# Optimization experiments

Hardware: AMD Instinct MI355X
Metric: run time of the kernel (lower is better)

Reference implementation:

```python
import jax, jax.numpy as jnp
import numpy as np

B, S, H, D = 2, 2048, 16, 64


def setup_inputs() -> dict:
    key = jax.random.key(0)
    kq, kk, kv, km = jax.random.split(key, 4)
    q = jax.random.normal(kq, (B, S, H, D), dtype=jnp.float32)
    k = jax.random.normal(kk, (B, S, H, D), dtype=jnp.float32)
    v = jax.random.normal(kv, (B, S, H, D), dtype=jnp.float32)
    pattern_mask = jax.random.bernoulli(km, 0.1, (S, S))
    return {"q": q, "k": k, "v": v, "pattern_mask": pattern_mask}


def reference(q, k, v, pattern_mask):
    # Faithful math of the torch module: for each query row i, attend only to
    # columns j where pattern_mask[i, j]; softmax over the selected columns
    # per (batch, head); rows with no selected columns produce zeros.
    head_dim = q.shape[-1]
    scale = 1.0 / jnp.sqrt(jnp.asarray(head_dim, dtype=q.dtype))
    # scores: [B, H, S_q, S_k]
    scores = jnp.einsum('bihd,bjhd->bhij', q, k) * scale
    neg = jnp.finfo(scores.dtype).min
    masked = jnp.where(pattern_mask[None, None, :, :], scores, neg)
    attn = jax.nn.softmax(masked, axis=-1)
    # zero out rows with no active columns (softmax over all-masked row is uniform garbage)
    row_has = jnp.any(pattern_mask, axis=-1)  # [S]
    attn = jnp.where(row_has[None, None, :, None], attn, jnp.zeros((), dtype=attn.dtype))
    # output: [B, S, H, D]
    out = jnp.einsum('bhij,bjhd->bihd', attn, v)
    return out
```

## Files before the change

### kernel.cpp

```cpp
#include <hip/hip_runtime.h>
#include <hip/hip_bf16.h>
#include <math.h>

#define SLEN 2048
#define NBATCH 2
#define NH 16
#define DH 64
#define WPR 64
#define NROUND 32
#define TILEB 16384
#define CONVBLK (NBATCH * NH * NROUND)
#define PACKBLK (SLEN * WPR / 256)

typedef __attribute__((ext_vector_type(4))) short short4v;
typedef __attribute__((ext_vector_type(8))) short short8v;
typedef __attribute__((ext_vector_type(4))) float float4v;
typedef __attribute__((ext_vector_type(16))) float float16v;

__device__ __forceinline__ unsigned short f2bf(float f) {
  unsigned u = __float_as_uint(f);
  u += 0x7fffu + ((u >> 16) & 1u);
  return (unsigned short)(u >> 16);
}

__device__ __forceinline__ float fexp2(float x) {
#if __has_builtin(__builtin_amdgcn_exp2f)
  return __builtin_amdgcn_exp2f(x);
#else
  return __expf(x * 0.6931471805599453f);
#endif
}

__device__ __forceinline__ unsigned pack_bf2(float a, float b) {
  unsigned ua = __float_as_uint(a); ua += 0x7fffu + ((ua >> 16) & 1u);
  unsigned ub = __float_as_uint(b); ub += 0x7fffu + ((ub >> 16) & 1u);
  return __builtin_amdgcn_perm(ub, ua, 0x07060302u);
}

__device__ __forceinline__ unsigned cvtpk(float lo, float hi) {
  unsigned r;
  asm("v_cvt_pk_bf16_f32 %0, %1, %2" : "=v"(r) : "v"(lo), "v"(hi));
  return r;
}

__device__ __forceinline__ unsigned nib4(unsigned w) {
  return ((w * 0x01020408u) >> 24) & 0xFu;
}

__global__ __launch_bounds__(256) void prep_kernel(
    const float* __restrict__ kk, const float* __restrict__ vv,
    const void* __restrict__ mask,
    char* __restrict__ img, unsigned* __restrict__ packed, int convblocks) {
  const int tid = threadIdx.x;
  if (blockIdx.x >= convblocks) {
    const int w = (blockIdx.x - convblocks) * 256 + tid;
    const uint4* bp = (const uint4*)((const char*)mask + (size_t)w * 32);
    uint4 x = bp[0], y = bp[1];
    const unsigned orw = (x.x | x.y) | (x.z | x.w) | (y.x | y.y) | (y.z | y.w);
    __shared__ int s0, sm;
    if (tid == 0) { s0 = 0; sm = 0; }
    __syncthreads();
    const int lane0 = ((tid & 63) == 0);
    if (__any((orw & 0x000000ffu) != 0) && lane0) atomicOr(&s0, 1);
    if (__any((orw & 0xffffff00u) != 0) && lane0) atomicOr(&sm, 1);
    __syncthreads();
    unsigned bits;
    if (s0 && sm) {
      bits = nib4(x.x) | (nib4(x.y) << 4) | (nib4(x.z) << 8) | (nib4(x.w) << 12) |
             (nib4(y.x) << 16) | (nib4(y.y) << 20) | (nib4(y.z) << 24) | (nib4(y.w) << 28);
    } else {
      const unsigned* m = (const unsigned*)mask + (size_t)w * 32;
      bits = 0u;
#pragma unroll
      for (int j = 0; j < 32; j++) bits |= (m[j] ? 1u : 0u) << j;
    }
    packed[w] = bits;
    return;
  }
  const int bid = blockIdx.x;
  const int t = bid & 31;
  const int bh = bid >> 5;
  const int b = bh >> 4, h = bh & 15;
  char* timg = img + (size_t)bid * TILEB;

  {
    const int r = tid >> 2;
    const int dg = (tid & 3) << 4;
    const float* src = kk + (((size_t)(b * SLEN + t * 64 + r) * NH + h) * DH + dg);
    const int f = ((r >> 5) << 2) + (dg >> 4);
    char* base = timg + f * 1024 + (r & 31) * 16;
    float4v x0 = *(const float4v*)(src);
    float4v x1 = *(const float4v*)(src + 4);
    float4v x2 = *(const float4v*)(src + 8);
    float4v x3 = *(const float4v*)(src + 12);
    union { unsigned u[4]; short8v s8; } lo, hi;
    lo.u[0] = pack_bf2(x0.x, x0.y); lo.u[1] = pack_bf2(x0.z, x0.w);
    lo.u[2] = pack_bf2(x1.x, x1.y); lo.u[3] = pack_bf2(x1.z, x1.w);
    hi.u[0] = pack_bf2(x2.x, x2.y); hi.u[1] = pack_bf2(x2.z, x2.w);
    hi.u[2] = pack_bf2(x3.x, x3.y); hi.u[3] = pack_bf2(x3.z, x3.w);
    *(short8v*)(base) = lo.s8;
    *(short8v*)(base + 512) = hi.s8;
  }
  {
    __shared__ unsigned short vlds[64 * 68];
    const int key = tid >> 2;
    const int dg = (tid & 3) << 4;
    const float* src = vv + (((size_t)(b * SLEN + t * 64 + key) * NH + h) * DH + dg);
    unsigned short* lp = vlds + key * 68 + dg;
#pragma unroll
    for (int i = 0; i < 4; i++) {
      float4v x = *(const float4v*)(src + i * 4);
      union { unsigned u[2]; short4v s4; } cv;
      cv.u[0] = pack_bf2(x.x, x.y);
      cv.u[1] = pack_bf2(x.z, x.w);
      *(short4v*)(lp + i * 4) = cv.s4;
    }
    __syncthreads();
#pragma unroll
    for (int c = 0; c < 2; c++) {
      const int cell = c * 256 + tid;
      const int fp = cell >> 6;
      const int lane16 = cell & 63;
      const int d = ((fp >> 2) & 1) * 32 + (lane16 & 31);
      const int pbase = 32 * ((fp >> 1) & 1) + 16 * (fp & 1) + 4 * (lane16 >> 5);
      union { unsigned short s[8]; short8v v8; } w;
#pragma unroll
      for (int slot = 0; slot < 8; slot++) {
        const int p = pbase + 8 * (slot >> 2) + (slot & 3);
        w.s[slot] = vlds[p * 68 + d];
      }
      *(short8v*)(timg + (8 + fp) * 1024 + lane16 * 16) = w.v8;
    }
  }
}

__global__ __launch_bounds__(256, 2) void sattn_fast13(
    const float* __restrict__ q, const unsigned* __restrict__ pmask,
    const char* __restrict__ img, float* __restrict__ out) {
  const int tid = threadIdx.x;
  const int xcd = blockIdx.x & 7;
  const int j = blockIdx.x >> 3;
  const int bh = xcd * 4 + (j >> 4);
  const int chunk = j & 15;
  const int b = bh >> 4;
  const int hd = bh & 15;
  const int wave = tid >> 6;
  const int lane = tid & 63;
  const int l31 = lane & 31;
  const int hl = lane >> 5;

  const int qrow = chunk * 128 + wave * 32 + l31;
  const int qw = qrow * WPR;

  const float SCL2 = 0.18033688011112042f;
  short8v qf[4];
  {
    const float* qp = q + (((size_t)b * SLEN + qrow) * NH + hd) * DH;
#pragma unroll
    for (int ds = 0; ds < 4; ds++) {
      float4v x0 = *(const float4v*)(qp + ds * 16 + hl * 8);
      float4v x1 = *(const float4v*)(qp + ds * 16 + hl * 8 + 4);
      union { unsigned u[4]; short8v s8; } cv;
      cv.u[0] = pack_bf2(x0.x * SCL2, x0.y * SCL2);
      cv.u[1] = pack_bf2(x0.z * SCL2, x0.w * SCL2);
      cv.u[2] = pack_bf2(x1.x * SCL2, x1.y * SCL2);
      cv.u[3] = pack_bf2(x1.z * SCL2, x1.w * SCL2);
      qf[ds] = cv.s8;
    }
  }

  const char* fb0 = img + (size_t)bh * (NROUND * TILEB) + lane * 16;
  const char* fb1 = fb0 + 4096;
  const char* fb2 = fb0 + 8192;
  const char* fb3 = fb0 + 12288;

  float16v acc0 = {}, acc1 = {};
  float lsum = 0.f;

  short8v kf0 = *(const short8v*)(fb0 + 0);
  short8v kf1 = *(const short8v*)(fb0 + 1024);
  short8v kf2 = *(const short8v*)(fb0 + 2048);
  short8v kf3 = *(const short8v*)(fb0 + 3072);
  short8v kf4 = *(const short8v*)(fb1 + 0);
  short8v kf5 = *(const short8v*)(fb1 + 1024);
  short8v kf6 = *(const short8v*)(fb1 + 2048);
  short8v kf7 = *(const short8v*)(fb1 + 3072);
  short8v vf0 = *(const short8v*)(fb2 + 0);
  short8v vf1 = *(const short8v*)(fb2 + 1024);
  short8v vf2 = *(const short8v*)(fb2 + 2048);
  short8v vf3 = *(const short8v*)(fb2 + 3072);
  short8v vf4 = *(const short8v*)(fb3 + 0);
  short8v vf5 = *(const short8v*)(fb3 + 1024);
  short8v vf6 = *(const short8v*)(fb3 + 2048);
  short8v vf7 = *(const short8v*)(fb3 + 3072);
  uint2 m = *(const uint2*)&pmask[qw];

  for (int t = 0; t < NROUND; t++) {
    const unsigned m0 = m.x, m1 = m.y;
    const int tn = (t + 1 < NROUND) ? t + 1 : t;

    __builtin_amdgcn_s_setprio(1);
    float16v st0 = {}, st1 = {};
    st0 = __builtin_amdgcn_mfma_f32_32x32x16_bf16(kf0, qf[0], st0, 0, 0, 0);
    st1 = __builtin_amdgcn_mfma_f32_32x32x16_bf16(kf4, qf[0], st1, 0, 0, 0);
    st0 = __builtin_amdgcn_mfma_f32_32x32x16_bf16(kf1, qf[1], st0, 0, 0, 0);
    st1 = __builtin_amdgcn_mfma_f32_32x32x16_bf16(kf5, qf[1], st1, 0, 0, 0);
    st0 = __builtin_amdgcn_mfma_f32_32x32x16_bf16(kf2, qf[2], st0, 0, 0, 0);
    st1 = __builtin_amdgcn_mfma_f32_32x32x16_bf16(kf6, qf[2], st1, 0, 0, 0);
    st0 = __builtin_amdgcn_mfma_f32_32x32x16_bf16(kf3, qf[3], st0, 0, 0, 0);
    st1 = __builtin_amdgcn_mfma_f32_32x32x16_bf16(kf7, qf[3], st1, 0, 0, 0);
    __builtin_amdgcn_s_setprio(0);

    const int adv = (tn != t) ? TILEB : 0;
    fb0 += adv; fb1 += adv; fb2 += adv; fb3 += adv;
    kf0 = *(const short8v*)(fb0 + 0);
    kf1 = *(const short8v*)(fb0 + 1024);
    kf2 = *(const short8v*)(fb0 + 2048);
    kf3 = *(const short8v*)(fb0 + 3072);
    kf4 = *(const short8v*)(fb1 + 0);
    kf5 = *(const short8v*)(fb1 + 1024);
    kf6 = *(const short8v*)(fb1 + 2048);
    kf7 = *(const short8v*)(fb1 + 3072);
    m = *(const uint2*)&pmask[qw + 2 * tn];

    float p0[16], p1[16];
#pragma unroll
    for (int u = 0; u < 4; u++) {
      const unsigned hw0 = m0 >> (8 * u + 4 * hl);
      const unsigned hw1 = m1 >> (8 * u + 4 * hl);
      {
        float a0 = fexp2(st0[4 * u + 0]); a0 = (hw0 & 1u) ? a0 : 0.f;
        float a1 = fexp2(st0[4 * u + 1]); a1 = (hw0 & 2u) ? a1 : 0.f;
        float a2 = fexp2(st0[4 * u + 2]); a2 = (hw0 & 4u) ? a2 : 0.f;
        float a3 = fexp2(st0[4 * u + 3]); a3 = (hw0 & 8u) ? a3 : 0.f;
        lsum += (a0 + a1) + (a2 + a3);
        p0[4 * u + 0] = a0; p0[4 * u + 1] = a1; p0[4 * u + 2] = a2; p0[4 * u + 3] = a3;
      }
      {
        float a0 = fexp2(st1[4 * u + 0]); a0 = (hw1 & 1u) ? a0 : 0.f;
        float a1 = fexp2(st1[4 * u + 1]); a1 = (hw1 & 2u) ? a1 : 0.f;
        float a2 = fexp2(st1[4 * u + 2]); a2 = (hw1 & 4u) ? a2 : 0.f;
        float a3 = fexp2(st1[4 * u + 3]); a3 = (hw1 & 8u) ? a3 : 0.f;
        lsum += (a0 + a1) + (a2 + a3);
        p1[4 * u + 0] = a0; p1[4 * u + 1] = a1; p1[4 * u + 2] = a2; p1[4 * u + 3] = a3;
      }
    }
    short8v pf0, pf1, pf2, pf3;
    {
      union { unsigned u[4]; short8v s8; } c0, c1, c2, c3;
#pragma unroll
      for (int jj = 0; jj < 4; jj++) {
        c0.u[jj] = cvtpk(p0[2 * jj], p0[2 * jj + 1]);
        c1.u[jj] = cvtpk(p0[8 + 2 * jj], p0[8 + 2 * jj + 1]);
        c2.u[jj] = cvtpk(p1[2 * jj], p1[2 * jj + 1]);
        c3.u[jj] = cvtpk(p1[8 + 2 * jj], p1[8 + 2 * jj + 1]);
      }
      pf0 = c0.s8; pf1 = c1.s8; pf2 = c2.s8; pf3 = c3.s8;
    }

    __builtin_amdgcn_s_setprio(1);
    acc0 = __builtin_amdgcn_mfma_f32_32x32x16_bf16(vf0, pf0, acc0, 0, 0, 0);
    acc1 = __builtin_amdgcn_mfma_f32_32x32x16_bf16(vf4, pf0, acc1, 0, 0, 0);
    acc0 = __builtin_amdgcn_mfma_f32_32x32x16_bf16(vf1, pf1, acc0, 0, 0, 0);
    acc1 = __builtin_amdgcn_mfma_f32_32x32x16_bf16(vf5, pf1, acc1, 0, 0, 0);
    acc0 = __builtin_amdgcn_mfma_f32_32x32x16_bf16(vf2, pf2, acc0, 0, 0, 0);
    acc1 = __builtin_amdgcn_mfma_f32_32x32x16_bf16(vf6, pf2, acc1, 0, 0, 0);
    acc0 = __builtin_amdgcn_mfma_f32_32x32x16_bf16(vf3, pf3, acc0, 0, 0, 0);
    acc1 = __builtin_amdgcn_mfma_f32_32x32x16_bf16(vf7, pf3, acc1, 0, 0, 0);
    __builtin_amdgcn_s_setprio(0);

    vf0 = *(const short8v*)(fb2 + 0);
    vf1 = *(const short8v*)(fb2 + 1024);
    vf2 = *(const short8v*)(fb2 + 2048);
    vf3 = *(const short8v*)(fb2 + 3072);
    vf4 = *(const short8v*)(fb3 + 0);
    vf5 = *(const short8v*)(fb3 + 1024);
    vf6 = *(const short8v*)(fb3 + 2048);
    vf7 = *(const short8v*)(fb3 + 3072);
  }

  lsum += __shfl_xor(lsum, 32);
  const float inv = (lsum > 0.f) ? 1.f / lsum : 0.f;
  float* op = out + (((size_t)b * SLEN + qrow) * NH + hd) * DH;
#pragma unroll
  for (int u = 0; u < 4; u++) {
    float4v o0, o1;
    o0.x = acc0[4 * u + 0] * inv; o0.y = acc0[4 * u + 1] * inv;
    o0.z = acc0[4 * u + 2] * inv; o0.w = acc0[4 * u + 3] * inv;
    o1.x = acc1[4 * u + 0] * inv; o1.y = acc1[4 * u + 1] * inv;
    o1.z = acc1[4 * u + 2] * inv; o1.w = acc1[4 * u + 3] * inv;
    *(float4v*)(op + 8 * u + 4 * hl) = o0;
    *(float4v*)(op + 32 + 8 * u + 4 * hl) = o1;
  }
}

__global__ __launch_bounds__(256) void sattn_fallback(
    const float* __restrict__ q, const float* __restrict__ kk,
    const float* __restrict__ vv, const unsigned int* __restrict__ pmask,
    float* __restrict__ out) {
  __shared__ __align__(16) unsigned short Kt[16 * 64];
  __shared__ __align__(16) unsigned short Vt[64 * 20];

  const int tid = threadIdx.x;
  const int chunk = blockIdx.x & 31;
  const int bh = blockIdx.x >> 5;
  const int b = bh >> 4;
  const int h = bh & 15;
  const int wave = tid >> 6;
  const int lane = tid & 63;
  const int lq = lane & 15;
  const int g = lane >> 4;

  const int qrow = chunk * 64 + wave * 16 + lq;

  short4v qf[4];
  {
    const float* qp = q + (((size_t)b * SLEN + qrow) * NH + h) * DH;
#pragma unroll
    for (int ks = 0; ks < 4; ks++) {
      float4v x = *(const float4v*)(qp + ks * 16 + g * 4);
      short4v s;
      s.x = (short)f2bf(x.x); s.y = (short)f2bf(x.y);
      s.z = (short)f2bf(x.z); s.w = (short)f2bf(x.w);
      qf[ks] = s;
    }
  }

  const int srow = tid >> 4;
  const int scol = (tid & 15) * 4;
  const size_t kvbase = (size_t)b * SLEN * (NH * DH) + (size_t)h * DH;

  float4v acc[4] = {};
  float m_run = -INFINITY;
  float l_run = 0.f;

  for (int t = 0; t < SLEN / 16; t++) {
    const int kbase = t * 16;
    __syncthreads();
    {
      const size_t rowoff = kvbase + (size_t)(kbase + srow) * (NH * DH) + scol;
      float4v x = *(const float4v*)(kk + rowoff);
      short4v s;
      s.x = (short)f2bf(x.x); s.y = (short)f2bf(x.y);
      s.z = (short)f2bf(x.z); s.w = (short)f2bf(x.w);
      const int off = (scol * 2) ^ ((srow & 7) << 4);
      *(short4v*)((char*)Kt + srow * 128 + off) = s;

      float4v y = *(const float4v*)(vv + rowoff);
      Vt[(scol + 0) * 20 + srow] = f2bf(y.x);
      Vt[(scol + 1) * 20 + srow] = f2bf(y.y);
      Vt[(scol + 2) * 20 + srow] = f2bf(y.z);
      Vt[(scol + 3) * 20 + srow] = f2bf(y.w);
    }
    __syncthreads();

    float4v stv = {0.f, 0.f, 0.f, 0.f};
#pragma unroll
    for (int ks = 0; ks < 4; ks++) {
      const int off = ((ks * 16 + g * 4) * 2) ^ ((lq & 7) << 4);
      short4v kf = *(const short4v*)((const char*)Kt + lq * 128 + off);
      stv = __builtin_amdgcn_mfma_f32_16x16x16bf16_1k(kf, qf[ks], stv, 0, 0, 0);
    }

    const unsigned int mw = pmask[qrow * WPR + (kbase >> 5)];
    const int shift = (kbase & 16) + g * 4;
    float sc[4];
    float tmax = -INFINITY;
#pragma unroll
    for (int r = 0; r < 4; r++) {
      bool a = (mw >> (shift + r)) & 1u;
      sc[r] = a ? stv[r] * 0.125f : -INFINITY;
      tmax = fmaxf(tmax, sc[r]);
    }
    tmax = fmaxf(tmax, __shfl_xor(tmax, 16));
    tmax = fmaxf(tmax, __shfl_xor(tmax, 32));
    const float mnew = fmaxf(m_run, tmax);
    const float muse = (mnew > -1e37f) ? mnew : 0.f;
    const float alpha = __expf(m_run - muse);
    float p[4], tsum = 0.f;
#pragma unroll
    for (int r = 0; r < 4; r++) {
      p[r] = __expf(sc[r] - muse);
      tsum += p[r];
    }
    tsum += __shfl_xor(tsum, 16);
    tsum += __shfl_xor(tsum, 32);
    l_run = l_run * alpha + tsum;
    m_run = mnew;

    short4v pfv;
    pfv.x = (short)f2bf(p[0]); pfv.y = (short)f2bf(p[1]);
    pfv.z = (short)f2bf(p[2]); pfv.w = (short)f2bf(p[3]);

#pragma unroll
    for (int n = 0; n < 4; n++) {
      acc[n][0] *= alpha; acc[n][1] *= alpha;
      acc[n][2] *= alpha; acc[n][3] *= alpha;
      short4v vf = *(const short4v*)((const char*)Vt + ((n * 16 + lq) * 20 + g * 4) * 2);
      acc[n] = __builtin_amdgcn_mfma_f32_16x16x16bf16_1k(vf, pfv, acc[n], 0, 0, 0);
    }
  }

  const float inv = (l_run > 0.f) ? 1.f / l_run : 0.f;
  float* op = out + (((size_t)b * SLEN + qrow) * NH + h) * DH;
#pragma unroll
  for (int n = 0; n < 4; n++) {
    float4v o;
    o.x = acc[n][0] * inv; o.y = acc[n][1] * inv;
    o.z = acc[n][2] * inv; o.w = acc[n][3] * inv;
    *(float4v*)(op + n * 16 + g * 4) = o;
  }
}

extern "C" void kernel_launch(void* const* d_in, const int* in_sizes, int n_in,
                              void* d_out, int out_size, void* d_ws, size_t ws_size,
                              hipStream_t stream) {
  const float* q = (const float*)d_in[0];
  const float* k = (const float*)d_in[1];
  const float* v = (const float*)d_in[2];
  const void* mask = d_in[3];
  float* out = (float*)d_out;

  unsigned int* packed = (unsigned int*)((char*)d_ws + 256);
  char* img = (char*)d_ws + (1 << 20);
  const size_t need = (size_t)(1 << 20) + (size_t)CONVBLK * TILEB;

  if (ws_size >= need) {
    prep_kernel<<<CONVBLK + PACKBLK, 256, 0, stream>>>(k, v, mask, img, packed, CONVBLK);
    sattn_fast13<<<NBATCH * NH * (SLEN / 128), 256, 0, stream>>>(q, packed, img, out);
  } else {
    prep_kernel<<<PACKBLK, 256, 0, stream>>>(k, v, mask, nullptr, packed, 0);
    sattn_fallback<<<NBATCH * NH * (SLEN / 64), 256, 0, stream>>>(q, k, v, packed, out);
  }
}
```

Measured before the change: 66.70 us.

## Stage K/V tiles in a shared LDS ring via async global-to-LDS loads

The attention kernel now runs 512-thread blocks that each cover 256 query rows. Previously every wave streamed its own copy of the pre-swizzled K/V tiles from global memory into registers. Now the whole block cooperatively copies groups of four tiles into a double-buffered 128KB LDS ring using direct global-to-LDS loads, and waves read their MFMA fragments from LDS. This cuts redundant L2/global traffic and overlaps the fetch of the next group with compute on the current one. The cost is a large LDS footprint that allows only one block per CU, a barrier per group, and LDS read latency that is no longer hidden by register prefetch. Whether the barrier waits for the async LDS loads depends on compiler-inserted waitcnts.

```diff
diff --git a/kernel.cpp b/kernel.cpp
--- a/kernel.cpp
+++ b/kernel.cpp
@@ -16,6 +16,9 @@
 typedef __attribute__((ext_vector_type(8))) short short8v;
 typedef __attribute__((ext_vector_type(4))) float float4v;
 typedef __attribute__((ext_vector_type(16))) float float16v;
+
+typedef __attribute__((address_space(1))) void gas_void;
+typedef __attribute__((address_space(3))) void las_void;
 
 __device__ __forceinline__ unsigned short f2bf(float f) {
   unsigned u = __float_as_uint(f);
@@ -134,14 +137,16 @@
   }
 }
 
-__global__ __launch_bounds__(256, 2) void sattn_fast13(
+__global__ __launch_bounds__(512, 2) void sattn_fast14(
     const float* __restrict__ q, const unsigned* __restrict__ pmask,
     const char* __restrict__ img, float* __restrict__ out) {
+  __shared__ __align__(16) char ring[8 * TILEB];
+
   const int tid = threadIdx.x;
   const int xcd = blockIdx.x & 7;
   const int j = blockIdx.x >> 3;
-  const int bh = xcd * 4 + (j >> 4);
-  const int chunk = j & 15;
+  const int bh = xcd * 4 + (j >> 3);
+  const int chunk = j & 7;
   const int b = bh >> 4;
   const int hd = bh & 15;
   const int wave = tid >> 6;
@@ -149,7 +154,7 @@
   const int l31 = lane & 31;
   const int hl = lane >> 5;
 
-  const int qrow = chunk * 128 + wave * 32 + l31;
+  const int qrow = chunk * 256 + wave * 32 + l31;
   const int qw = qrow * WPR;
 
   const float SCL2 = 0.18033688011112042f;
@@ -169,114 +174,118 @@
     }
   }
 
-  const char* fb0 = img + (size_t)bh * (NROUND * TILEB) + lane * 16;
-  const char* fb1 = fb0 + 4096;
-  const char* fb2 = fb0 + 8192;
-  const char* fb3 = fb0 + 12288;
+  const char* gimg = img + (size_t)bh * (NROUND * TILEB) + tid * 16;
 
   float16v acc0 = {}, acc1 = {};
   float lsum = 0.f;
 
-  short8v kf0 = *(const short8v*)(fb0 + 0);
-  short8v kf1 = *(const short8v*)(fb0 + 1024);
-  short8v kf2 = *(const short8v*)(fb0 + 2048);
-  short8v kf3 = *(const short8v*)(fb0 + 3072);
-  short8v kf4 = *(const short8v*)(fb1 + 0);
-  short8v kf5 = *(const short8v*)(fb1 + 1024);
-  short8v kf6 = *(const short8v*)(fb1 + 2048);
-  short8v kf7 = *(const short8v*)(fb1 + 3072);
-  short8v vf0 = *(const short8v*)(fb2 + 0);
-  short8v vf1 = *(const short8v*)(fb2 + 1024);
-  short8v vf2 = *(const short8v*)(fb2 + 2048);
-  short8v vf3 = *(const short8v*)(fb2 + 3072);
-  short8v vf4 = *(const short8v*)(fb3 + 0);
-  short8v vf5 = *(const short8v*)(fb3 + 1024);
-  short8v vf6 = *(const short8v*)(fb3 + 2048);
-  short8v vf7 = *(const short8v*)(fb3 + 3072);
-  uint2 m = *(const uint2*)&pmask[qw];
-
-  for (int t = 0; t < NROUND; t++) {
-    const unsigned m0 = m.x, m1 = m.y;
-    const int tn = (t + 1 < NROUND) ? t + 1 : t;
-
-    __builtin_amdgcn_s_setprio(1);
-    float16v st0 = {}, st1 = {};
-    st0 = __builtin_amdgcn_mfma_f32_32x32x16_bf16(kf0, qf[0], st0, 0, 0, 0);
-    st1 = __builtin_amdgcn_mfma_f32_32x32x16_bf16(kf4, qf[0], st1, 0, 0, 0);
-    st0 = __builtin_amdgcn_mfma_f32_32x32x16_bf16(kf1, qf[1], st0, 0, 0, 0);
-    st1 = __builtin_amdgcn_mfma_f32_32x32x16_bf16(kf5, qf[1], st1, 0, 0, 0);
-    st0 = __builtin_amdgcn_mfma_f32_32x32x16_bf16(kf2, qf[2], st0, 0, 0, 0);
-    st1 = __builtin_amdgcn_mfma_f32_32x32x16_bf16(kf6, qf[2], st1, 0, 0, 0);
-    st0 = __builtin_amdgcn_mfma_f32_32x32x16_bf16(kf3, qf[3], st0, 0, 0, 0);
-    st1 = __builtin_amdgcn_mfma_f32_32x32x16_bf16(kf7, qf[3], st1, 0, 0, 0);
-    __builtin_amdgcn_s_setprio(0);
-
-    const int adv = (tn != t) ? TILEB : 0;
-    fb0 += adv; fb1 += adv; fb2 += adv; fb3 += adv;
-    kf0 = *(const short8v*)(fb0 + 0);
-    kf1 = *(const short8v*)(fb0 + 1024);
-    kf2 = *(const short8v*)(fb0 + 2048);
-    kf3 = *(const short8v*)(fb0 + 3072);
-    kf4 = *(const short8v*)(fb1 + 0);
-    kf5 = *(const short8v*)(fb1 + 1024);
-    kf6 = *(const short8v*)(fb1 + 2048);
-    kf7 = *(const short8v*)(fb1 + 3072);
-    m = *(const uint2*)&pmask[qw + 2 * tn];
-
-    float p0[16], p1[16];
+#pragma unroll
+  for (int i = 0; i < 4; i++) {
+    char* dst = &ring[i * TILEB] + tid * 16;
+    const char* src = gimg + (size_t)i * TILEB;
+    __builtin_amdgcn_global_load_lds((gas_void*)(src), (las_void*)(dst), 16, 0, 0);
+    __builtin_amdgcn_global_load_lds((gas_void*)(src + 8192), (las_void*)(dst + 8192), 16, 0, 0);
+  }
+  __syncthreads();
+
+  for (int g = 0; g < 8; g++) {
+    if (g < 7) {
+      const int dstbase = ((g + 1) & 1) * 4;
+#pragma unroll
+      for (int i = 0; i < 4; i++) {
+        const int tn = 4 * g + 4 + i;
+        char* dst = &ring[(dstbase + i) * TILEB] + tid * 16;
+        const char* src = gimg + (size_t)tn * TILEB;
+        __builtin_amdgcn_global_load_lds((gas_void*)(src), (las_void*)(dst), 16, 0, 0);
+        __builtin_amdgcn_global_load_lds((gas_void*)(src + 8192), (las_void*)(dst + 8192), 16, 0, 0);
+      }
+    }
+
 #pragma unroll
     for (int u = 0; u < 4; u++) {
-      const unsigned hw0 = m0 >> (8 * u + 4 * hl);
-      const unsigned hw1 = m1 >> (8 * u + 4 * hl);
+      const int t = 4 * g + u;
+      const char* Kl = &ring[((g & 1) * 4 + u) * TILEB] + lane * 16;
+      const char* Vl = Kl + 8192;
+      const uint2 m = *(const uint2*)&pmask[qw + 2 * t];
+      const unsigned m0 = m.x, m1 = m.y;
+
+      short8v kf0 = *(const short8v*)(Kl + 0);
+      short8v kf1 = *(const short8v*)(Kl + 1024);
+      short8v kf2 = *(const short8v*)(Kl + 2048);
+      short8v kf3 = *(const short8v*)(Kl + 3072);
+      short8v kf4 = *(const short8v*)(Kl + 4096);
+      short8v kf5 = *(const short8v*)(Kl + 5120);
+      short8v kf6 = *(const short8v*)(Kl + 6144);
+      short8v kf7 = *(const short8v*)(Kl + 7168);
+
+      __builtin_amdgcn_s_setprio(1);
+      float16v st0 = {}, st1 = {};
+      st0 = __builtin_amdgcn_mfma_f32_32x32x16_bf16(kf0, qf[0], st0, 0, 0, 0);
+      st1 = __builtin_amdgcn_mfma_f32_32x32x16_bf16(kf4, qf[0], st1, 0, 0, 0);
+      st0 = __builtin_amdgcn_mfma_f32_32x32x16_bf16(kf1, qf[1], st0, 0, 0, 0);
+      st1 = __builtin_amdgcn_mfma_f32_32x32x16_bf16(kf5, qf[1], st1, 0, 0, 0);
+      st0 = __builtin_amdgcn_mfma_f32_32x32x16_bf16(kf2, qf[2], st0, 0, 0, 0);
+      st1 = __builtin_amdgcn_mfma_f32_32x32x16_bf16(kf6, qf[2], st1, 0, 0, 0);
+      st0 = __builtin_amdgcn_mfma_f32_32x32x16_bf16(kf3, qf[3], st0, 0, 0, 0);
+      st1 = __builtin_amdgcn_mfma_f32_32x32x16_bf16(kf7, qf[3], st1, 0, 0, 0);
+      __builtin_amdgcn_s_setprio(0);
+
+      float p0[16], p1[16];
+#pragma unroll
+      for (int uu = 0; uu < 4; uu++) {
+        const unsigned hw0 = m0 >> (8 * uu + 4 * hl);
+        const unsigned hw1 = m1 >> (8 * uu + 4 * hl);
+        {
+          float a0 = fexp2(st0[4 * uu + 0]); a0 = (hw0 & 1u) ? a0 : 0.f;
+          float a1 = fexp2(st0[4 * uu + 1]); a1 = (hw0 & 2u) ? a1 : 0.f;
+          float a2 = fexp2(st0[4 * uu + 2]); a2 = (hw0 & 4u) ? a2 : 0.f;
+          float a3 = fexp2(st0[4 * uu + 3]); a3 = (hw0 & 8u) ? a3 : 0.f;
+          lsum += (a0 + a1) + (a2 + a3);
+          p0[4 * uu + 0] = a0; p0[4 * uu + 1] = a1; p0[4 * uu + 2] = a2; p0[4 * uu + 3] = a3;
+        }
+        {
+          float a0 = fexp2(st1[4 * uu + 0]); a0 = (hw1 & 1u) ? a0 : 0.f;
+          float a1 = fexp2(st1[4 * uu + 1]); a1 = (hw1 & 2u) ? a1 : 0.f;
+          float a2 = fexp2(st1[4 * uu + 2]); a2 = (hw1 & 4u) ? a2 : 0.f;
+          float a3 = fexp2(st1[4 * uu + 3]); a3 = (hw1 & 8u) ? a3 : 0.f;
+          lsum += (a0 + a1) + (a2 + a3);
+          p1[4 * uu + 0] = a0; p1[4 * uu + 1] = a1; p1[4 * uu + 2] = a2; p1[4 * uu + 3] = a3;
+        }
+      }
+      short8v pf0, pf1, pf2, pf3;
       {
-        float a0 = fexp2(st0[4 * u + 0]); a0 = (hw0 & 1u) ? a0 : 0.f;
-        float a1 = fexp2(st0[4 * u + 1]); a1 = (hw0 & 2u) ? a1 : 0.f;
-        float a2 = fexp2(st0[4 * u + 2]); a2 = (hw0 & 4u) ? a2 : 0.f;
-        float a3 = fexp2(st0[4 * u + 3]); a3 = (hw0 & 8u) ? a3 : 0.f;
-        lsum += (a0 + a1) + (a2 + a3);
-        p0[4 * u + 0] = a0; p0[4 * u + 1] = a1; p0[4 * u + 2] = a2; p0[4 * u + 3] = a3;
+        union { unsigned u[4]; short8v s8; } c0, c1, c2, c3;
+#pragma unroll
+        for (int jj = 0; jj < 4; jj++) {
+          c0.u[jj] = cvtpk(p0[2 * jj], p0[2 * jj + 1]);
+          c1.u[jj] = cvtpk(p0[8 + 2 * jj], p0[8 + 2 * jj + 1]);
+          c2.u[jj] = cvtpk(p1[2 * jj], p1[2 * jj + 1]);
+          c3.u[jj] = cvtpk(p1[8 + 2 * jj], p1[8 + 2 * jj + 1]);
+        }
+        pf0 = c0.s8; pf1 = c1.s8; pf2 = c2.s8; pf3 = c3.s8;
       }
-      {
-        float a0 = fexp2(st1[4 * u + 0]); a0 = (hw1 & 1u) ? a0 : 0.f;
-        float a1 = fexp2(st1[4 * u + 1]); a1 = (hw1 & 2u) ? a1 : 0.f;
-        float a2 = fexp2(st1[4 * u + 2]); a2 = (hw1 & 4u) ? a2 : 0.f;
-        float a3 = fexp2(st1[4 * u + 3]); a3 = (hw1 & 8u) ? a3 : 0.f;
-        lsum += (a0 + a1) + (a2 + a3);
-        p1[4 * u + 0] = a0; p1[4 * u + 1] = a1; p1[4 * u + 2] = a2; p1[4 * u + 3] = a3;
-      }
-    }
-    short8v pf0, pf1, pf2, pf3;
-    {
-      union { unsigned u[4]; short8v s8; } c0, c1, c2, c3;
-#pragma unroll
-      for (int jj = 0; jj < 4; jj++) {
-        c0.u[jj] = cvtpk(p0[2 * jj], p0[2 * jj + 1]);
-        c1.u[jj] = cvtpk(p0[8 + 2 * jj], p0[8 + 2 * jj + 1]);
-        c2.u[jj] = cvtpk(p1[2 * jj], p1[2 * jj + 1]);
-        c3.u[jj] = cvtpk(p1[8 + 2 * jj], p1[8 + 2 * jj + 1]);
-      }
-      pf0 = c0.s8; pf1 = c1.s8; pf2 = c2.s8; pf3 = c3.s8;
-    }
-
-    __builtin_amdgcn_s_setprio(1);
-    acc0 = __builtin_amdgcn_mfma_f32_32x32x16_bf16(vf0, pf0, acc0, 0, 0, 0);
-    acc1 = __builtin_amdgcn_mfma_f32_32x32x16_bf16(vf4, pf0, acc1, 0, 0, 0);
-    acc0 = __builtin_amdgcn_mfma_f32_32x32x16_bf16(vf1, pf1, acc0, 0, 0, 0);
-    acc1 = __builtin_amdgcn_mfma_f32_32x32x16_bf16(vf5, pf1, acc1, 0, 0, 0);
-    acc0 = __builtin_amdgcn_mfma_f32_32x32x16_bf16(vf2, pf2, acc0, 0, 0, 0);
-    acc1 = __builtin_amdgcn_mfma_f32_32x32x16_bf16(vf6, pf2, acc1, 0, 0, 0);
-    acc0 = __builtin_amdgcn_mfma_f32_32x32x16_bf16(vf3, pf3, acc0, 0, 0, 0);
-    acc1 = __builtin_amdgcn_mfma_f32_32x32x16_bf16(vf7, pf3, acc1, 0, 0, 0);
-    __builtin_amdgcn_s_setprio(0);
-
-    vf0 = *(const short8v*)(fb2 + 0);
-    vf1 = *(const short8v*)(fb2 + 1024);
-    vf2 = *(const short8v*)(fb2 + 2048);
-    vf3 = *(const short8v*)(fb2 + 3072);
-    vf4 = *(const short8v*)(fb3 + 0);
-    vf5 = *(const short8v*)(fb3 + 1024);
-    vf6 = *(const short8v*)(fb3 + 2048);
-    vf7 = *(const short8v*)(fb3 + 3072);
+
+      short8v vf0 = *(const short8v*)(Vl + 0);
+      short8v vf1 = *(const short8v*)(Vl + 1024);
+      short8v vf2 = *(const short8v*)(Vl + 2048);
+      short8v vf3 = *(const short8v*)(Vl + 3072);
+      short8v vf4 = *(const short8v*)(Vl + 4096);
+      short8v vf5 = *(const short8v*)(Vl + 5120);
+      short8v vf6 = *(const short8v*)(Vl + 6144);
+      short8v vf7 = *(const short8v*)(Vl + 7168);
+      __builtin_amdgcn_s_setprio(1);
+      acc0 = __builtin_amdgcn_mfma_f32_32x32x16_bf16(vf0, pf0, acc0, 0, 0, 0);
+      acc1 = __builtin_amdgcn_mfma_f32_32x32x16_bf16(vf4, pf0, acc1, 0, 0, 0);
+      acc0 = __builtin_amdgcn_mfma_f32_32x32x16_bf16(vf1, pf1, acc0, 0, 0, 0);
+      acc1 = __builtin_amdgcn_mfma_f32_32x32x16_bf16(vf5, pf1, acc1, 0, 0, 0);
+      acc0 = __builtin_amdgcn_mfma_f32_32x32x16_bf16(vf2, pf2, acc0, 0, 0, 0);
+      acc1 = __builtin_amdgcn_mfma_f32_32x32x16_bf16(vf6, pf2, acc1, 0, 0, 0);
+      acc0 = __builtin_amdgcn_mfma_f32_32x32x16_bf16(vf3, pf3, acc0, 0, 0, 0);
+      acc1 = __builtin_amdgcn_mfma_f32_32x32x16_bf16(vf7, pf3, acc1, 0, 0, 0);
+      __builtin_amdgcn_s_setprio(0);
+    }
+
+    __syncthreads();
   }
 
   lsum += __shfl_xor(lsum, 32);
@@ -427,7 +436,7 @@
 
   if (ws_size >= need) {
     prep_kernel<<<CONVBLK + PACKBLK, 256, 0, stream>>>(k, v, mask, img, packed, CONVBLK);
-    sattn_fast13<<<NBATCH * NH * (SLEN / 128), 256, 0, stream>>>(q, packed, img, out);
+    sattn_fast14<<<NBATCH * NH * (SLEN / 256), 512, 0, stream>>>(q, packed, img, out);
   } else {
     prep_kernel<<<PACKBLK, 256, 0, stream>>>(k, v, mask, nullptr, packed, 0);
     sattn_fallback<<<NBATCH * NH * (SLEN / 64), 256, 0, stream>>>(q, k, v, packed, out);
```

Result: no change. 66.04 us (median of 2 runs) (-1.0%).
